# Kernel tuning notes

Hardware: AMD Instinct MI355X
Metric: run time of the kernel (lower is better)

Reference implementation:

```python
import jax, jax.numpy as jnp
import numpy as np
import math

M, N, D, P = 512, 4096, 128, 4096
H = N // D

def setup_inputs() -> dict:
    key = jax.random.key(0)
    k1, k2, k3, k4, k5 = jax.random.split(key, 5)
    return {
        "X": jax.random.normal(k1, (M, N), dtype=jnp.float32),
        "weight": jnp.ones((N,), dtype=jnp.float32),
        "W": jax.random.normal(k2, (3 * N, N), dtype=jnp.float32) * (1.0 / math.sqrt(N)),
        "q": jax.random.normal(k3, (H, M, D), dtype=jnp.float32),
        "cache_K": jax.random.normal(k4, (H, P, D), dtype=jnp.float32),
        "cache_V": jax.random.normal(k5, (H, P, D), dtype=jnp.float32),
    }

def reference(X, weight, W, q, cache_K, cache_V):
    d = q.shape[-1]
    scale = 1.0 / math.sqrt(d)
    # RMSNorm over last dim (matches F.rms_norm default eps = dtype eps)
    eps = jnp.finfo(X.dtype).eps
    X_norm = X * jax.lax.rsqrt(jnp.mean(X * X, axis=-1, keepdims=True) + eps) * weight
    # QKV projection (computed in the original forward; output unused by attention)
    qkv = X_norm @ W.T  # [M, 3N]
    del qkv
    # Batched multi-head cached-KV attention (replaces per-head Python loop)
    scores = jnp.einsum('hmd,hpd->hmp', q, cache_K) * scale  # [H, M, P]
    attn = jax.nn.softmax(scores, axis=-1)
    out = jnp.einsum('hmp,hpd->hmd', attn, cache_V)  # [H, M, D]
    # concat heads along last dim -> [M, H*D]
    Hh, Mm, Dd = out.shape
    return jnp.transpose(out, (1, 0, 2)).reshape(Mm, Hh * Dd)
```

## Files before the change

### kernel.cpp

```cpp
#include <hip/hip_runtime.h>
#include <hip/hip_bf16.h>


#define NH   32
#define MQ   512
#define DD   128
#define PKV  4096
#define QBLK 64
#define KVB  64
#define NIT  (PKV / KVB)
#define VSTR 68

typedef float  f32x4  __attribute__((ext_vector_type(4)));
typedef __bf16 bf16x4 __attribute__((ext_vector_type(4)));
typedef __bf16 bf16x8 __attribute__((ext_vector_type(8)));

__global__ __launch_bounds__(256, 1)
void attn_fused_kernel(const float* __restrict__ qg,
                       const float* __restrict__ kg,
                       const float* __restrict__ vg,
                       float* __restrict__ outg)
{
    __shared__ __align__(16) __bf16 k_lds[KVB * DD];
    __shared__ __align__(16) __bf16 vt_lds[DD * VSTR];

    const int tid  = threadIdx.x;
    const int lane = tid & 63;
    const int w    = tid >> 6;
    const int q16  = lane & 15;
    const int hi   = lane >> 4;

    const int bx = blockIdx.x;
    const int h  = bx & 31;
    const int qt = bx >> 5;

    const float SCL = 0.08838834764831845f * 1.4426950408889634f;
    const int rowq = qt * QBLK + w * 16 + q16;
    const float* qrow = qg + ((size_t)h * MQ + rowq) * DD;
    bf16x8 qf[4];
#pragma unroll
    for (int ks = 0; ks < 4; ++ks) {
        const float* p = qrow + ks * 32 + hi * 8;
        f32x4 a = *(const f32x4*)(p);
        f32x4 b = *(const f32x4*)(p + 4);
#pragma unroll
        for (int c = 0; c < 4; ++c) {
            qf[ks][c]     = (__bf16)(a[c] * SCL);
            qf[ks][c + 4] = (__bf16)(b[c] * SCL);
        }
    }

    const int srow = tid >> 5;
    const int scol = (tid & 31) * 4;
    const float* kbase = kg + (size_t)h * PKV * DD;
    const float* vbase = vg + (size_t)h * PKV * DD;

    f32x4 kreg[8], vreg[8];
#pragma unroll
    for (int j = 0; j < 8; ++j) {
        size_t off = (size_t)(8 * j + srow) * DD + scol;
        kreg[j] = *(const f32x4*)(kbase + off);
        vreg[j] = *(const f32x4*)(vbase + off);
    }

    f32x4 o[8];
#pragma unroll
    for (int dt = 0; dt < 8; ++dt) o[dt] = (f32x4){0.f, 0.f, 0.f, 0.f};
    float m_run = -1e30f;
    float l_run = 0.f;

    for (int it = 0; it < NIT; ++it) {
        __syncthreads();
#pragma unroll
        for (int j = 0; j < 8; ++j) {
            int kv = 8 * j + srow;
            bf16x4 pk;
#pragma unroll
            for (int c = 0; c < 4; ++c) pk[c] = (__bf16)kreg[j][c];
            int idx = kv * DD + (scol ^ ((kv & 7) << 3));
            *(bf16x4*)&k_lds[idx] = pk;
#pragma unroll
            for (int c = 0; c < 4; ++c)
                vt_lds[(scol + c) * VSTR + kv] = (__bf16)vreg[j][c];
        }
        __syncthreads();

        if (it + 1 < NIT) {
            const float* kb = kbase + (size_t)(it + 1) * KVB * DD;
            const float* vb = vbase + (size_t)(it + 1) * KVB * DD;
#pragma unroll
            for (int j = 0; j < 8; ++j) {
                size_t off = (size_t)(8 * j + srow) * DD + scol;
                kreg[j] = *(const f32x4*)(kb + off);
                vreg[j] = *(const f32x4*)(vb + off);
            }
        }

        f32x4 st[4];
#pragma unroll
        for (int t = 0; t < 4; ++t) st[t] = (f32x4){0.f, 0.f, 0.f, 0.f};
#pragma unroll
        for (int ks = 0; ks < 4; ++ks) {
#pragma unroll
            for (int t = 0; t < 4; ++t) {
                int kvrow = t * 16 + q16;
                int d0 = ks * 32 + hi * 8;
                bf16x8 kf = *(const bf16x8*)&k_lds[kvrow * DD + (d0 ^ ((kvrow & 7) << 3))];
                st[t] = __builtin_amdgcn_mfma_f32_16x16x32_bf16(kf, qf[ks], st[t], 0, 0, 0);
            }
        }

        float mt = st[0][0];
#pragma unroll
        for (int t = 0; t < 4; ++t)
#pragma unroll
            for (int r = 0; r < 4; ++r) mt = fmaxf(mt, st[t][r]);
        mt = fmaxf(mt, __shfl_xor(mt, 16));
        mt = fmaxf(mt, __shfl_xor(mt, 32));
        float m_new = fmaxf(m_run, mt);
        float alpha = __builtin_amdgcn_exp2f(m_run - m_new);

        float lsum = 0.f;
        bf16x8 pa[2];
#pragma unroll
        for (int t = 0; t < 4; ++t) {
#pragma unroll
            for (int r = 0; r < 4; ++r) {
                float pv = __builtin_amdgcn_exp2f(st[t][r] - m_new);
                lsum += pv;
                pa[t >> 1][(t & 1) * 4 + r] = (__bf16)pv;
            }
        }
        lsum += __shfl_xor(lsum, 16);
        lsum += __shfl_xor(lsum, 32);
        l_run = l_run * alpha + lsum;
        m_run = m_new;

        f32x4 av;
#pragma unroll
        for (int r = 0; r < 4; ++r) av[r] = __shfl(alpha, hi * 4 + r);
#pragma unroll
        for (int dt = 0; dt < 8; ++dt)
#pragma unroll
            for (int r = 0; r < 4; ++r) o[dt][r] *= av[r];

#pragma unroll
        for (int c = 0; c < 2; ++c) {
#pragma unroll
            for (int dt = 0; dt < 8; ++dt) {
                int idx = (dt * 16 + q16) * VSTR + c * 32 + hi * 4;
                bf16x4 v0 = *(const bf16x4*)&vt_lds[idx];
                bf16x4 v1 = *(const bf16x4*)&vt_lds[idx + 16];
                bf16x8 vf;
#pragma unroll
                for (int e = 0; e < 4; ++e) { vf[e] = v0[e]; vf[e + 4] = v1[e]; }
                o[dt] = __builtin_amdgcn_mfma_f32_16x16x32_bf16(pa[c], vf, o[dt], 0, 0, 0);
            }
        }
    }

    f32x4 linv;
#pragma unroll
    for (int r = 0; r < 4; ++r) linv[r] = 1.0f / __shfl(l_run, hi * 4 + r);
    const int row0 = qt * QBLK + w * 16;
#pragma unroll
    for (int dt = 0; dt < 8; ++dt) {
#pragma unroll
        for (int r = 0; r < 4; ++r) {
            int row = row0 + hi * 4 + r;
            int col = h * DD + dt * 16 + q16;
            outg[(size_t)row * (NH * DD) + col] = o[dt][r] * linv[r];
        }
    }
}

extern "C" void kernel_launch(void* const* d_in, const int* in_sizes, int n_in,
                              void* d_out, int out_size, void* d_ws, size_t ws_size,
                              hipStream_t stream) {
    (void)in_sizes; (void)n_in; (void)d_ws; (void)ws_size; (void)out_size;
    const float* q  = (const float*)d_in[3];
    const float* ck = (const float*)d_in[4];
    const float* cv = (const float*)d_in[5];
    float* out = (float*)d_out;
    attn_fused_kernel<<<dim3(NH * (MQ / QBLK)), dim3(256), 0, stream>>>(q, ck, cv, out);
}
```

Before: 451.1 us.

## Split KV sequence across blocks with partial softmax combine kernel

Splits the KV length into four chunks per head and query tile, so each block writes unnormalized partial outputs and running max/sum to the workspace. A second kernel merges the partials with log-sum-exp weights. This raises block count and occupancy (launch bounds changed to allow 4 blocks per CU). It also rotates the transposed V layout in LDS to reduce bank conflicts and raises wave priority around MFMA sections. It adds extra global traffic for partials and a second launch, and it falls back to the single-pass path if the workspace is too small.

```diff
diff --git a/kernel.cpp b/kernel.cpp
--- a/kernel.cpp
+++ b/kernel.cpp
@@ -8,18 +8,22 @@
 #define PKV  4096
 #define QBLK 64
 #define KVB  64
-#define NIT  (PKV / KVB)
 #define VSTR 68
+#define PSPLIT 4
+#define NROW (NH * MQ)
 
 typedef float  f32x4  __attribute__((ext_vector_type(4)));
 typedef __bf16 bf16x4 __attribute__((ext_vector_type(4)));
 typedef __bf16 bf16x8 __attribute__((ext_vector_type(8)));
 
-__global__ __launch_bounds__(256, 1)
-void attn_fused_kernel(const float* __restrict__ qg,
-                       const float* __restrict__ kg,
-                       const float* __restrict__ vg,
-                       float* __restrict__ outg)
+__global__ __launch_bounds__(256, 4)
+void attn_pass1(const float* __restrict__ qg,
+                const float* __restrict__ kg,
+                const float* __restrict__ vg,
+                float* __restrict__ outg,
+                float* __restrict__ opart,
+                float* __restrict__ mlpart,
+                int ngshift, int nit, int partial)
 {
     __shared__ __align__(16) __bf16 k_lds[KVB * DD];
     __shared__ __align__(16) __bf16 vt_lds[DD * VSTR];
@@ -31,8 +35,11 @@
     const int hi   = lane >> 4;
 
     const int bx = blockIdx.x;
-    const int h  = bx & 31;
-    const int qt = bx >> 5;
+    const int g  = bx & ((1 << ngshift) - 1);
+    const int qt = bx >> ngshift;
+    const int h  = g & 31;
+    const int p  = g >> 5;
+    const int kvbase = p * nit * KVB;
 
     const float SCL = 0.08838834764831845f * 1.4426950408889634f;
     const int rowq = qt * QBLK + w * 16 + q16;
@@ -40,9 +47,9 @@
     bf16x8 qf[4];
 #pragma unroll
     for (int ks = 0; ks < 4; ++ks) {
-        const float* p = qrow + ks * 32 + hi * 8;
-        f32x4 a = *(const f32x4*)(p);
-        f32x4 b = *(const f32x4*)(p + 4);
+        const float* ptr = qrow + ks * 32 + hi * 8;
+        f32x4 a = *(const f32x4*)(ptr);
+        f32x4 b = *(const f32x4*)(ptr + 4);
 #pragma unroll
         for (int c = 0; c < 4; ++c) {
             qf[ks][c]     = (__bf16)(a[c] * SCL);
@@ -51,9 +58,11 @@
     }
 
     const int srow = tid >> 5;
-    const int scol = (tid & 31) * 4;
-    const float* kbase = kg + (size_t)h * PKV * DD;
-    const float* vbase = vg + (size_t)h * PKV * DD;
+    const int ii   = tid & 31;
+    const int scol = ii * 4;
+    const int vrot = 4 * (ii & 15);
+    const float* kbase = kg + ((size_t)h * PKV + kvbase) * DD;
+    const float* vbase = vg + ((size_t)h * PKV + kvbase) * DD;
 
     f32x4 kreg[8], vreg[8];
 #pragma unroll
@@ -69,7 +78,7 @@
     float m_run = -1e30f;
     float l_run = 0.f;
 
-    for (int it = 0; it < NIT; ++it) {
+    for (int it = 0; it < nit; ++it) {
         __syncthreads();
 #pragma unroll
         for (int j = 0; j < 8; ++j) {
@@ -79,13 +88,14 @@
             for (int c = 0; c < 4; ++c) pk[c] = (__bf16)kreg[j][c];
             int idx = kv * DD + (scol ^ ((kv & 7) << 3));
             *(bf16x4*)&k_lds[idx] = pk;
+            int kvr = (kv + vrot) & 63;
 #pragma unroll
             for (int c = 0; c < 4; ++c)
-                vt_lds[(scol + c) * VSTR + kv] = (__bf16)vreg[j][c];
+                vt_lds[(scol + c) * VSTR + kvr] = (__bf16)vreg[j][c];
         }
         __syncthreads();
 
-        if (it + 1 < NIT) {
+        if (it + 1 < nit) {
             const float* kb = kbase + (size_t)(it + 1) * KVB * DD;
             const float* vb = vbase + (size_t)(it + 1) * KVB * DD;
 #pragma unroll
@@ -99,6 +109,7 @@
         f32x4 st[4];
 #pragma unroll
         for (int t = 0; t < 4; ++t) st[t] = (f32x4){0.f, 0.f, 0.f, 0.f};
+        __builtin_amdgcn_s_setprio(1);
 #pragma unroll
         for (int ks = 0; ks < 4; ++ks) {
 #pragma unroll
@@ -109,6 +120,7 @@
                 st[t] = __builtin_amdgcn_mfma_f32_16x16x32_bf16(kf, qf[ks], st[t], 0, 0, 0);
             }
         }
+        __builtin_amdgcn_s_setprio(0);
 
         float mt = st[0][0];
 #pragma unroll
@@ -144,43 +156,115 @@
 #pragma unroll
             for (int r = 0; r < 4; ++r) o[dt][r] *= av[r];
 
+        __builtin_amdgcn_s_setprio(1);
 #pragma unroll
         for (int c = 0; c < 2; ++c) {
 #pragma unroll
             for (int dt = 0; dt < 8; ++dt) {
-                int idx = (dt * 16 + q16) * VSTR + c * 32 + hi * 4;
-                bf16x4 v0 = *(const bf16x4*)&vt_lds[idx];
-                bf16x4 v1 = *(const bf16x4*)&vt_lds[idx + 16];
+                int drow = dt * 16 + q16;
+                int rot = (16 * dt + 4 * (q16 >> 2)) & 63;
+                int kb0 = (c * 32 + hi * 4 + rot) & 63;
+                int kb1 = (c * 32 + hi * 4 + 16 + rot) & 63;
+                bf16x4 v0 = *(const bf16x4*)&vt_lds[drow * VSTR + kb0];
+                bf16x4 v1 = *(const bf16x4*)&vt_lds[drow * VSTR + kb1];
                 bf16x8 vf;
 #pragma unroll
                 for (int e = 0; e < 4; ++e) { vf[e] = v0[e]; vf[e + 4] = v1[e]; }
                 o[dt] = __builtin_amdgcn_mfma_f32_16x16x32_bf16(pa[c], vf, o[dt], 0, 0, 0);
             }
         }
-    }
-
-    f32x4 linv;
-#pragma unroll
-    for (int r = 0; r < 4; ++r) linv[r] = 1.0f / __shfl(l_run, hi * 4 + r);
+        __builtin_amdgcn_s_setprio(0);
+    }
+
     const int row0 = qt * QBLK + w * 16;
-#pragma unroll
-    for (int dt = 0; dt < 8; ++dt) {
-#pragma unroll
-        for (int r = 0; r < 4; ++r) {
-            int row = row0 + hi * 4 + r;
-            int col = h * DD + dt * 16 + q16;
-            outg[(size_t)row * (NH * DD) + col] = o[dt][r] * linv[r];
-        }
-    }
+    if (partial) {
+        const int rbase = h * MQ + row0;
+        float* ob = opart + ((size_t)p * NROW + rbase) * DD;
+#pragma unroll
+        for (int dt = 0; dt < 8; ++dt)
+#pragma unroll
+            for (int r = 0; r < 4; ++r)
+                ob[(size_t)(hi * 4 + r) * DD + dt * 16 + q16] = o[dt][r];
+        if (lane < 16) {
+            size_t mi = ((size_t)p * NROW + rbase + lane) * 2;
+            mlpart[mi]     = m_run;
+            mlpart[mi + 1] = l_run;
+        }
+    } else {
+        f32x4 linv;
+#pragma unroll
+        for (int r = 0; r < 4; ++r) linv[r] = 1.0f / __shfl(l_run, hi * 4 + r);
+#pragma unroll
+        for (int dt = 0; dt < 8; ++dt) {
+#pragma unroll
+            for (int r = 0; r < 4; ++r) {
+                int row = row0 + hi * 4 + r;
+                int col = h * DD + dt * 16 + q16;
+                outg[(size_t)row * (NH * DD) + col] = o[dt][r] * linv[r];
+            }
+        }
+    }
+}
+
+__global__ __launch_bounds__(256)
+void attn_combine(const float* __restrict__ opart,
+                  const float* __restrict__ mlpart,
+                  float* __restrict__ outg)
+{
+    int idx = blockIdx.x * 256 + threadIdx.x;
+    int r = idx >> 5;
+    int c = idx & 31;
+
+    float m[PSPLIT], l[PSPLIT];
+#pragma unroll
+    for (int p2 = 0; p2 < PSPLIT; ++p2) {
+        size_t mi = ((size_t)p2 * NROW + r) * 2;
+        m[p2] = mlpart[mi];
+        l[p2] = mlpart[mi + 1];
+    }
+    float mstar = m[0];
+#pragma unroll
+    for (int p2 = 1; p2 < PSPLIT; ++p2) mstar = fmaxf(mstar, m[p2]);
+
+    float denom = 0.f;
+    f32x4 acc = (f32x4){0.f, 0.f, 0.f, 0.f};
+#pragma unroll
+    for (int p2 = 0; p2 < PSPLIT; ++p2) {
+        float wgt = __builtin_amdgcn_exp2f(m[p2] - mstar);
+        denom += wgt * l[p2];
+        f32x4 ov = *(const f32x4*)&opart[(((size_t)p2 * NROW + r) << 7) + c * 4];
+#pragma unroll
+        for (int e = 0; e < 4; ++e) acc[e] += wgt * ov[e];
+    }
+    float dinv = 1.0f / denom;
+    int mrow = r & 511;
+    int hh   = r >> 9;
+    f32x4 res;
+#pragma unroll
+    for (int e = 0; e < 4; ++e) res[e] = acc[e] * dinv;
+    *(f32x4*)&outg[(size_t)mrow * (NH * DD) + hh * DD + c * 4] = res;
 }
 
 extern "C" void kernel_launch(void* const* d_in, const int* in_sizes, int n_in,
                               void* d_out, int out_size, void* d_ws, size_t ws_size,
                               hipStream_t stream) {
-    (void)in_sizes; (void)n_in; (void)d_ws; (void)ws_size; (void)out_size;
+    (void)in_sizes; (void)n_in; (void)out_size;
     const float* q  = (const float*)d_in[3];
     const float* ck = (const float*)d_in[4];
     const float* cv = (const float*)d_in[5];
     float* out = (float*)d_out;
-    attn_fused_kernel<<<dim3(NH * (MQ / QBLK)), dim3(256), 0, stream>>>(q, ck, cv, out);
+
+    const size_t needO  = (size_t)PSPLIT * NROW * DD * sizeof(float);
+    const size_t needML = (size_t)PSPLIT * NROW * 2 * sizeof(float);
+
+    if (ws_size >= needO + needML) {
+        float* opart = (float*)d_ws;
+        float* ml    = (float*)((char*)d_ws + needO);
+        attn_pass1<<<dim3(NH * PSPLIT * (MQ / QBLK)), dim3(256), 0, stream>>>(
+            q, ck, cv, nullptr, opart, ml, 7, PKV / PSPLIT / KVB, 1);
+        attn_combine<<<dim3(NROW * 32 / 256), dim3(256), 0, stream>>>(opart, ml, out);
+    } else {
+        attn_pass1<<<dim3(NH * (MQ / QBLK)), dim3(256), 0, stream>>>(
+            q, ck, cv, out, nullptr, nullptr, 5, PKV / KVB, 0);
+    }
 }
```

Result: slower. 648.6 us (+43.8%).
